# Kernel optimization log

Measured on AMD Instinct MI355X. Metric: run time of the kernel, lower is better.

Reference implementation:

```python
import jax, jax.numpy as jnp
import numpy as np

EMBED_DIM = 128
NUM_HEADS = 16
D_K = EMBED_DIM // NUM_HEADS  # 8 qubits per head
DEPTH = 2

# Sign matrix for PauliZ expectations: wire w corresponds to bit (D_K-1-w) of the
# flattened state index (wire 0 = most significant axis, torchquantum convention).
_idx = np.arange(2 ** D_K)
_SIGNS = np.stack([1.0 - 2.0 * ((_idx >> (D_K - 1 - w)) & 1) for w in range(D_K)], axis=1).astype(np.float32)  # [2^d_k, d_k]


def quantum_layer(tokens, qparams):
    """Simulate the variational circuit for a batch of tokens.
    tokens: [N, d_k] real angles; qparams: [depth, d_k] trainable RX angles.
    RX(a)RX(b)=RX(a+b) on the same wire, so encoder + all depth RX layers
    compose into a single RX per wire. Then `depth` CNOT ladders, then <Z_w>.
    """
    theta = tokens + jnp.sum(qparams, axis=0)  # [N, d_k]
    half = 0.5 * theta
    # single-qubit amplitudes after RX(theta)|0>: [cos(t/2), -i sin(t/2)]
    amp = jnp.stack([jnp.cos(half).astype(jnp.complex64),
                     (-1j) * jnp.sin(half).astype(jnp.complex64)], axis=-1)  # [N, d_k, 2]
    # build product state [N, 2, 2, ..., 2]
    state = amp[:, 0, :]
    for i in range(1, D_K):
        state = jnp.einsum('n...,nq->n...q', state, amp[:, i, :])
    # depth x CNOT ladder: CNOT(i, i+1) for i in 0..d_k-2
    for _ in range(DEPTH):
        for i in range(D_K - 1):
            c_ax = 1 + i
            c0 = jnp.take(state, 0, axis=c_ax)
            c1 = jnp.take(state, 1, axis=c_ax)
            c1 = jnp.flip(c1, axis=c_ax)  # target axis = c_ax+1, shifted by -1 after take
            state = jnp.stack([c0, c1], axis=c_ax)
    probs = (state.real ** 2 + state.imag ** 2).reshape(state.shape[0], -1)  # [N, 2^d_k]
    return probs @ jnp.asarray(_SIGNS)  # [N, d_k]


def setup_inputs() -> dict:
    key = jax.random.key(0)
    ks = jax.random.split(key, 6)
    B, S, E = 4, 512, EMBED_DIM
    scale = 1.0 / np.sqrt(E)
    return {
        'x': jax.random.normal(ks[0], (B, S, E), dtype=jnp.float32),
        'Wq': jax.random.normal(ks[1], (E, E), dtype=jnp.float32) * scale,
        'Wk': jax.random.normal(ks[2], (E, E), dtype=jnp.float32) * scale,
        'Wv': jax.random.normal(ks[3], (E, E), dtype=jnp.float32) * scale,
        'Wo': jax.random.normal(ks[4], (E, E), dtype=jnp.float32) * scale,
        'qparams': jax.random.normal(ks[5], (DEPTH, D_K), dtype=jnp.float32),
    }


def reference(x, Wq, Wk, Wv, Wo, qparams):
    B, S, E = x.shape
    H, dk = NUM_HEADS, D_K
    # linear projections (torch Linear, no bias): y = x @ W.T
    q = (x @ Wq.T).reshape(B, S, H, dk).transpose(0, 2, 1, 3)  # [B,H,S,dk]
    k = (x @ Wk.T).reshape(B, S, H, dk).transpose(0, 2, 1, 3)
    v = (x @ Wv.T).reshape(B, S, H, dk).transpose(0, 2, 1, 3)
    # batched quantum circuit over all (batch, head, seq) tokens; shared weights
    qq = quantum_layer(q.reshape(-1, dk), qparams).reshape(B, H, S, dk)
    kq = quantum_layer(k.reshape(-1, dk), qparams).reshape(B, H, S, dk)
    vq = quantum_layer(v.reshape(-1, dk), qparams).reshape(B, H, S, dk)
    scores = jnp.einsum('bhqd,bhkd->bhqk', qq, kq) / jnp.sqrt(jnp.float32(dk))
    attn = jax.nn.softmax(scores, axis=-1)  # dropout in eval mode: identity
    out = jnp.einsum('bhqk,bhkd->bhqd', attn, vq)
    out = out.transpose(0, 2, 1, 3).reshape(B, S, E)
    return out @ Wo.T
```

## Files before the change

kernel.cpp:

```cpp
#include <hip/hip_runtime.h>
#include <cmath>

#define MATSZ 262144
#define WT_OFF 0
#define QKV_OFF 65536
#define AOUT_OFF (65536 + 3 * MATSZ)

__global__ __launch_bounds__(256) void k_prep(
    const float* __restrict__ Wq, const float* __restrict__ Wk,
    const float* __restrict__ Wv, const float* __restrict__ Wo,
    float* __restrict__ ws) {
  __shared__ float s[32][33];
  const int m = blockIdx.y;
  const int tr = blockIdx.x >> 2;
  const int tc = blockIdx.x & 3;
  const float* W = (m == 0) ? Wq : (m == 1) ? Wk : (m == 2) ? Wv : Wo;
  const int lk = threadIdx.x & 31;
  const int l0 = threadIdx.x >> 5;
#pragma unroll
  for (int i = 0; i < 4; ++i) {
    int lc = l0 + i * 8;
    s[lc][lk] = W[(size_t)(tr * 32 + lc) * 128 + tc * 32 + lk];
  }
  __syncthreads();
  float* wt = ws + WT_OFF + m * 16384;
#pragma unroll
  for (int i = 0; i < 4; ++i) {
    int lkk = l0 + i * 8;
    wt[(size_t)(tc * 32 + lkk) * 128 + tr * 32 + lk] = s[lk][lkk];
  }
}

__global__ __launch_bounds__(256, 4) void k_qkvq(
    const float* __restrict__ x, const float* __restrict__ qp,
    float* __restrict__ ws) {
  __shared__ float xs[8][128];
  __shared__ float th[8][128];
  const int t = threadIdx.x;
  const int tile = blockIdx.x;
  const int m = blockIdx.y;
  {
    const float4* xg = (const float4*)(x + (size_t)tile * 1024);
    ((float4*)&xs[0][0])[t] = xg[t];
  }
  __syncthreads();
  const int cg = t & 31, rg = t >> 5;
  const float4* wt4 = (const float4*)(ws + WT_OFF + m * 16384);
  const float* xr = &xs[rg][0];
  float4 acc = make_float4(0.f, 0.f, 0.f, 0.f);
#pragma unroll 8
  for (int k = 0; k < 128; ++k) {
    float4 w = wt4[k * 32 + cg];
    float xv = xr[k];
    acc.x = fmaf(xv, w.x, acc.x);
    acc.y = fmaf(xv, w.y, acc.y);
    acc.z = fmaf(xv, w.z, acc.z);
    acc.w = fmaf(xv, w.w, acc.w);
  }
  const int j0 = (cg & 1) * 4;
  float4 cc;
  cc.x = __cosf(acc.x + qp[j0 + 0] + qp[8 + j0 + 0]);
  cc.y = __cosf(acc.y + qp[j0 + 1] + qp[8 + j0 + 1]);
  cc.z = __cosf(acc.z + qp[j0 + 2] + qp[8 + j0 + 2]);
  cc.w = __cosf(acc.w + qp[j0 + 3] + qp[8 + j0 + 3]);
  ((float4*)&th[rg][0])[cg] = cc;
  __syncthreads();
  if (t < 128) {
    const int r = t >> 4, h = t & 15;
    const float* tb = &th[r][h * 8];
    float o0 = tb[0], o1 = tb[1];
    float o2 = o0 * tb[2], o3 = o1 * tb[3];
    float o4 = o2 * tb[4], o5 = o3 * tb[5];
    float o6 = o4 * tb[6], o7 = o5 * tb[7];
    int row = tile * 8 + r;
    int b = row >> 9, s = row & 511;
    float* dst = ws + QKV_OFF + (size_t)m * MATSZ +
                 ((size_t)((b << 4) + h) * 512 + s) * 8;
    ((float4*)dst)[0] = make_float4(o0, o1, o2, o3);
    ((float4*)dst)[1] = make_float4(o4, o5, o6, o7);
  }
}

__global__ __launch_bounds__(256, 4) void k_attn(
    float* __restrict__ ws) {
  __shared__ float4 kslo[512], kshi[512], vslo[512], vshi[512];
  const int qt = blockIdx.x;
  const int bh = blockIdx.y;
  const float* qkv = ws + QKV_OFF;
  const float* Qg = qkv + (size_t)bh * 4096;
  const float4* Kg = (const float4*)(qkv + MATSZ + (size_t)bh * 4096);
  const float4* Vg = (const float4*)(qkv + 2 * (size_t)MATSZ + (size_t)bh * 4096);
  const int t = threadIdx.x;
  for (int k = t; k < 512; k += 256) {
    kslo[k] = Kg[2 * k]; kshi[k] = Kg[2 * k + 1];
    vslo[k] = Vg[2 * k]; vshi[k] = Vg[2 * k + 1];
  }
  __syncthreads();
  const int qslot = t >> 4, ko = t & 15;
  const int row0 = qt * 32 + qslot * 2;
  const float scale = 0.35355339059327373f;
  float4 qa0 = ((const float4*)(Qg + (size_t)row0 * 8))[0];
  float4 qb0 = ((const float4*)(Qg + (size_t)row0 * 8))[1];
  float4 qa1 = ((const float4*)(Qg + (size_t)(row0 + 1) * 8))[0];
  float4 qb1 = ((const float4*)(Qg + (size_t)(row0 + 1) * 8))[1];
  qa0.x *= scale; qa0.y *= scale; qa0.z *= scale; qa0.w *= scale;
  qb0.x *= scale; qb0.y *= scale; qb0.z *= scale; qb0.w *= scale;
  qa1.x *= scale; qa1.y *= scale; qa1.z *= scale; qa1.w *= scale;
  qb1.x *= scale; qb1.y *= scale; qb1.z *= scale; qb1.w *= scale;
  float l0 = 0.f, l1 = 0.f;
  float a0[8] = {0.f, 0.f, 0.f, 0.f, 0.f, 0.f, 0.f, 0.f};
  float a1[8] = {0.f, 0.f, 0.f, 0.f, 0.f, 0.f, 0.f, 0.f};
#pragma unroll 2
  for (int i = 0; i < 32; ++i) {
    int k = i * 16 + ko;
    float4 kx = kslo[k], ky = kshi[k];
    float s0 = qa0.x * kx.x + qa0.y * kx.y + qa0.z * kx.z + qa0.w * kx.w +
               qb0.x * ky.x + qb0.y * ky.y + qb0.z * ky.z + qb0.w * ky.w;
    float s1 = qa1.x * kx.x + qa1.y * kx.y + qa1.z * kx.z + qa1.w * kx.w +
               qb1.x * ky.x + qb1.y * ky.y + qb1.z * ky.z + qb1.w * ky.w;
    float p0 = __expf(s0), p1 = __expf(s1);
    float4 vx = vslo[k], vy = vshi[k];
    l0 += p0; l1 += p1;
    a0[0] = fmaf(p0, vx.x, a0[0]); a1[0] = fmaf(p1, vx.x, a1[0]);
    a0[1] = fmaf(p0, vx.y, a0[1]); a1[1] = fmaf(p1, vx.y, a1[1]);
    a0[2] = fmaf(p0, vx.z, a0[2]); a1[2] = fmaf(p1, vx.z, a1[2]);
    a0[3] = fmaf(p0, vx.w, a0[3]); a1[3] = fmaf(p1, vx.w, a1[3]);
    a0[4] = fmaf(p0, vy.x, a0[4]); a1[4] = fmaf(p1, vy.x, a1[4]);
    a0[5] = fmaf(p0, vy.y, a0[5]); a1[5] = fmaf(p1, vy.y, a1[5]);
    a0[6] = fmaf(p0, vy.z, a0[6]); a1[6] = fmaf(p1, vy.z, a1[6]);
    a0[7] = fmaf(p0, vy.w, a0[7]); a1[7] = fmaf(p1, vy.w, a1[7]);
  }
#pragma unroll
  for (int mm = 1; mm <= 8; mm <<= 1) {
    l0 += __shfl_xor(l0, mm);
    l1 += __shfl_xor(l1, mm);
#pragma unroll
    for (int j = 0; j < 8; ++j) {
      a0[j] += __shfl_xor(a0[j], mm);
      a1[j] += __shfl_xor(a1[j], mm);
    }
  }
  if (ko == 0) {
    float i0 = 1.f / l0, i1 = 1.f / l1;
    int b = bh >> 4, h = bh & 15;
    float* aout = ws + AOUT_OFF;
    float* d0 = aout + ((size_t)(b * 512 + row0)) * 128 + h * 8;
    ((float4*)d0)[0] = make_float4(a0[0] * i0, a0[1] * i0, a0[2] * i0, a0[3] * i0);
    ((float4*)d0)[1] = make_float4(a0[4] * i0, a0[5] * i0, a0[6] * i0, a0[7] * i0);
    float* d1 = d0 + 128;
    ((float4*)d1)[0] = make_float4(a1[0] * i1, a1[1] * i1, a1[2] * i1, a1[3] * i1);
    ((float4*)d1)[1] = make_float4(a1[4] * i1, a1[5] * i1, a1[6] * i1, a1[7] * i1);
  }
}

__global__ __launch_bounds__(256, 4) void k_out(
    const float* __restrict__ ws, float* __restrict__ out) {
  __shared__ float as_[4][128];
  const int t = threadIdx.x;
  const int tile = blockIdx.x;
  const float* aout = ws + AOUT_OFF;
  if (t < 128)
    ((float4*)&as_[0][0])[t] = ((const float4*)(aout + (size_t)tile * 512))[t];
  __syncthreads();
  const int cg = t & 63, rg = t >> 6;
  const float2* wt2 = (const float2*)(ws + WT_OFF + 3 * 16384);
  const float* ar = &as_[rg][0];
  float2 acc = make_float2(0.f, 0.f);
#pragma unroll 8
  for (int k = 0; k < 128; ++k) {
    float2 w = wt2[k * 64 + cg];
    float xv = ar[k];
    acc.x = fmaf(xv, w.x, acc.x);
    acc.y = fmaf(xv, w.y, acc.y);
  }
  ((float2*)(out + (size_t)(tile * 4 + rg) * 128))[cg] = acc;
}

extern "C" void kernel_launch(void* const* d_in, const int* in_sizes, int n_in,
                              void* d_out, int out_size, void* d_ws, size_t ws_size,
                              hipStream_t stream) {
  const float* x  = (const float*)d_in[0];
  const float* Wq = (const float*)d_in[1];
  const float* Wk = (const float*)d_in[2];
  const float* Wv = (const float*)d_in[3];
  const float* Wo = (const float*)d_in[4];
  const float* qp = (const float*)d_in[5];
  float* out = (float*)d_out;
  float* ws = (float*)d_ws;

  hipLaunchKernelGGL(k_prep, dim3(16, 4), dim3(256), 0, stream,
                     Wq, Wk, Wv, Wo, ws);
  hipLaunchKernelGGL(k_qkvq, dim3(256, 3), dim3(256), 0, stream, x, qp, ws);
  hipLaunchKernelGGL(k_attn, dim3(16, 64), dim3(256), 0, stream, ws);
  hipLaunchKernelGGL(k_out, dim3(512), dim3(256), 0, stream, ws, out);
}
```

Before: 49.33 us.

## Increase per-thread row blocking in projection, attention and output kernels

The QKV projection and output projection kernels now have each thread compute two rows with float4 x/weight reads, so each weight load is reused across rows and each block handles 16 rows. The quantum product chain is now computed in registers, with a lane shuffle replacing the shared-memory staging and second barrier. Attention threads now process four query rows instead of two, so K/V shared-memory reads are amortized over more rows. Grids shrink (128x3, 8x64, 128), which cuts redundant K/V staging but lowers parallelism and raises register pressure.

```diff
diff --git a/kernel.cpp b/kernel.cpp
--- a/kernel.cpp
+++ b/kernel.cpp
@@ -34,50 +34,75 @@
 __global__ __launch_bounds__(256, 4) void k_qkvq(
     const float* __restrict__ x, const float* __restrict__ qp,
     float* __restrict__ ws) {
-  __shared__ float xs[8][128];
-  __shared__ float th[8][128];
+  __shared__ float xs[16][128];
   const int t = threadIdx.x;
   const int tile = blockIdx.x;
   const int m = blockIdx.y;
   {
-    const float4* xg = (const float4*)(x + (size_t)tile * 1024);
-    ((float4*)&xs[0][0])[t] = xg[t];
+    const float4* xg = (const float4*)(x + (size_t)tile * 2048);
+    float4* xv = (float4*)&xs[0][0];
+    xv[t] = xg[t];
+    xv[t + 256] = xg[t + 256];
   }
   __syncthreads();
   const int cg = t & 31, rg = t >> 5;
   const float4* wt4 = (const float4*)(ws + WT_OFF + m * 16384);
-  const float* xr = &xs[rg][0];
-  float4 acc = make_float4(0.f, 0.f, 0.f, 0.f);
-#pragma unroll 8
-  for (int k = 0; k < 128; ++k) {
-    float4 w = wt4[k * 32 + cg];
-    float xv = xr[k];
-    acc.x = fmaf(xv, w.x, acc.x);
-    acc.y = fmaf(xv, w.y, acc.y);
-    acc.z = fmaf(xv, w.z, acc.z);
-    acc.w = fmaf(xv, w.w, acc.w);
+  const float4* xs4 = (const float4*)&xs[0][0];
+  float4 acc0 = make_float4(0.f, 0.f, 0.f, 0.f);
+  float4 acc1 = make_float4(0.f, 0.f, 0.f, 0.f);
+#pragma unroll 4
+  for (int kc = 0; kc < 32; ++kc) {
+    float4 w0 = wt4[(kc * 4 + 0) * 32 + cg];
+    float4 w1 = wt4[(kc * 4 + 1) * 32 + cg];
+    float4 w2 = wt4[(kc * 4 + 2) * 32 + cg];
+    float4 w3 = wt4[(kc * 4 + 3) * 32 + cg];
+    float4 xa = xs4[(rg * 2 + 0) * 32 + kc];
+    float4 xb = xs4[(rg * 2 + 1) * 32 + kc];
+    acc0.x = fmaf(xa.x, w0.x, acc0.x); acc0.y = fmaf(xa.x, w0.y, acc0.y);
+    acc0.z = fmaf(xa.x, w0.z, acc0.z); acc0.w = fmaf(xa.x, w0.w, acc0.w);
+    acc0.x = fmaf(xa.y, w1.x, acc0.x); acc0.y = fmaf(xa.y, w1.y, acc0.y);
+    acc0.z = fmaf(xa.y, w1.z, acc0.z); acc0.w = fmaf(xa.y, w1.w, acc0.w);
+    acc0.x = fmaf(xa.z, w2.x, acc0.x); acc0.y = fmaf(xa.z, w2.y, acc0.y);
+    acc0.z = fmaf(xa.z, w2.z, acc0.z); acc0.w = fmaf(xa.z, w2.w, acc0.w);
+    acc0.x = fmaf(xa.w, w3.x, acc0.x); acc0.y = fmaf(xa.w, w3.y, acc0.y);
+    acc0.z = fmaf(xa.w, w3.z, acc0.z); acc0.w = fmaf(xa.w, w3.w, acc0.w);
+    acc1.x = fmaf(xb.x, w0.x, acc1.x); acc1.y = fmaf(xb.x, w0.y, acc1.y);
+    acc1.z = fmaf(xb.x, w0.z, acc1.z); acc1.w = fmaf(xb.x, w0.w, acc1.w);
+    acc1.x = fmaf(xb.y, w1.x, acc1.x); acc1.y = fmaf(xb.y, w1.y, acc1.y);
+    acc1.z = fmaf(xb.y, w1.z, acc1.z); acc1.w = fmaf(xb.y, w1.w, acc1.w);
+    acc1.x = fmaf(xb.z, w2.x, acc1.x); acc1.y = fmaf(xb.z, w2.y, acc1.y);
+    acc1.z = fmaf(xb.z, w2.z, acc1.z); acc1.w = fmaf(xb.z, w2.w, acc1.w);
+    acc1.x = fmaf(xb.w, w3.x, acc1.x); acc1.y = fmaf(xb.w, w3.y, acc1.y);
+    acc1.z = fmaf(xb.w, w3.z, acc1.z); acc1.w = fmaf(xb.w, w3.w, acc1.w);
   }
   const int j0 = (cg & 1) * 4;
-  float4 cc;
-  cc.x = __cosf(acc.x + qp[j0 + 0] + qp[8 + j0 + 0]);
-  cc.y = __cosf(acc.y + qp[j0 + 1] + qp[8 + j0 + 1]);
-  cc.z = __cosf(acc.z + qp[j0 + 2] + qp[8 + j0 + 2]);
-  cc.w = __cosf(acc.w + qp[j0 + 3] + qp[8 + j0 + 3]);
-  ((float4*)&th[rg][0])[cg] = cc;
-  __syncthreads();
-  if (t < 128) {
-    const int r = t >> 4, h = t & 15;
-    const float* tb = &th[r][h * 8];
-    float o0 = tb[0], o1 = tb[1];
-    float o2 = o0 * tb[2], o3 = o1 * tb[3];
-    float o4 = o2 * tb[4], o5 = o3 * tb[5];
-    float o6 = o4 * tb[6], o7 = o5 * tb[7];
-    int row = tile * 8 + r;
+  float4 qs;
+  qs.x = qp[j0 + 0] + qp[8 + j0 + 0];
+  qs.y = qp[j0 + 1] + qp[8 + j0 + 1];
+  qs.z = qp[j0 + 2] + qp[8 + j0 + 2];
+  qs.w = qp[j0 + 3] + qp[8 + j0 + 3];
+  const int h = cg >> 1;
+  const bool hi = (cg & 1) != 0;
+#pragma unroll
+  for (int r = 0; r < 2; ++r) {
+    float4 a = (r == 0) ? acc0 : acc1;
+    float4 c;
+    c.x = __cosf(a.x + qs.x);
+    c.y = __cosf(a.y + qs.y);
+    c.z = __cosf(a.z + qs.z);
+    c.w = __cosf(a.w + qs.w);
+    float4 u;
+    u.x = c.x; u.y = c.y; u.z = c.x * c.z; u.w = c.y * c.w;
+    float gz = __shfl_xor(u.z, 1);
+    float gw = __shfl_xor(u.w, 1);
+    float mz = hi ? gz : 1.f, mw = hi ? gw : 1.f;
+    float4 o;
+    o.x = u.x * mz; o.y = u.y * mw; o.z = u.z * mz; o.w = u.w * mw;
+    int row = tile * 16 + rg * 2 + r;
     int b = row >> 9, s = row & 511;
     float* dst = ws + QKV_OFF + (size_t)m * MATSZ +
-                 ((size_t)((b << 4) + h) * 512 + s) * 8;
-    ((float4*)dst)[0] = make_float4(o0, o1, o2, o3);
-    ((float4*)dst)[1] = make_float4(o4, o5, o6, o7);
+                 ((size_t)((b << 4) + h) * 512 + s) * 8 + (hi ? 4 : 0);
+    *(float4*)dst = o;
   }
 }
 
@@ -97,83 +122,113 @@
   }
   __syncthreads();
   const int qslot = t >> 4, ko = t & 15;
-  const int row0 = qt * 32 + qslot * 2;
+  const int row0 = qt * 64 + qslot * 4;
   const float scale = 0.35355339059327373f;
-  float4 qa0 = ((const float4*)(Qg + (size_t)row0 * 8))[0];
-  float4 qb0 = ((const float4*)(Qg + (size_t)row0 * 8))[1];
-  float4 qa1 = ((const float4*)(Qg + (size_t)(row0 + 1) * 8))[0];
-  float4 qb1 = ((const float4*)(Qg + (size_t)(row0 + 1) * 8))[1];
-  qa0.x *= scale; qa0.y *= scale; qa0.z *= scale; qa0.w *= scale;
-  qb0.x *= scale; qb0.y *= scale; qb0.z *= scale; qb0.w *= scale;
-  qa1.x *= scale; qa1.y *= scale; qa1.z *= scale; qa1.w *= scale;
-  qb1.x *= scale; qb1.y *= scale; qb1.z *= scale; qb1.w *= scale;
-  float l0 = 0.f, l1 = 0.f;
-  float a0[8] = {0.f, 0.f, 0.f, 0.f, 0.f, 0.f, 0.f, 0.f};
-  float a1[8] = {0.f, 0.f, 0.f, 0.f, 0.f, 0.f, 0.f, 0.f};
+  float4 qa[4], qb[4];
+#pragma unroll
+  for (int r = 0; r < 4; ++r) {
+    qa[r] = ((const float4*)(Qg + (size_t)(row0 + r) * 8))[0];
+    qb[r] = ((const float4*)(Qg + (size_t)(row0 + r) * 8))[1];
+    qa[r].x *= scale; qa[r].y *= scale; qa[r].z *= scale; qa[r].w *= scale;
+    qb[r].x *= scale; qb[r].y *= scale; qb[r].z *= scale; qb[r].w *= scale;
+  }
+  float l[4] = {0.f, 0.f, 0.f, 0.f};
+  float a[4][8];
+#pragma unroll
+  for (int r = 0; r < 4; ++r)
+#pragma unroll
+    for (int j = 0; j < 8; ++j) a[r][j] = 0.f;
 #pragma unroll 2
   for (int i = 0; i < 32; ++i) {
     int k = i * 16 + ko;
     float4 kx = kslo[k], ky = kshi[k];
-    float s0 = qa0.x * kx.x + qa0.y * kx.y + qa0.z * kx.z + qa0.w * kx.w +
-               qb0.x * ky.x + qb0.y * ky.y + qb0.z * ky.z + qb0.w * ky.w;
-    float s1 = qa1.x * kx.x + qa1.y * kx.y + qa1.z * kx.z + qa1.w * kx.w +
-               qb1.x * ky.x + qb1.y * ky.y + qb1.z * ky.z + qb1.w * ky.w;
-    float p0 = __expf(s0), p1 = __expf(s1);
     float4 vx = vslo[k], vy = vshi[k];
-    l0 += p0; l1 += p1;
-    a0[0] = fmaf(p0, vx.x, a0[0]); a1[0] = fmaf(p1, vx.x, a1[0]);
-    a0[1] = fmaf(p0, vx.y, a0[1]); a1[1] = fmaf(p1, vx.y, a1[1]);
-    a0[2] = fmaf(p0, vx.z, a0[2]); a1[2] = fmaf(p1, vx.z, a1[2]);
-    a0[3] = fmaf(p0, vx.w, a0[3]); a1[3] = fmaf(p1, vx.w, a1[3]);
-    a0[4] = fmaf(p0, vy.x, a0[4]); a1[4] = fmaf(p1, vy.x, a1[4]);
-    a0[5] = fmaf(p0, vy.y, a0[5]); a1[5] = fmaf(p1, vy.y, a1[5]);
-    a0[6] = fmaf(p0, vy.z, a0[6]); a1[6] = fmaf(p1, vy.z, a1[6]);
-    a0[7] = fmaf(p0, vy.w, a0[7]); a1[7] = fmaf(p1, vy.w, a1[7]);
+#pragma unroll
+    for (int r = 0; r < 4; ++r) {
+      float s = qa[r].x * kx.x + qa[r].y * kx.y + qa[r].z * kx.z + qa[r].w * kx.w +
+                qb[r].x * ky.x + qb[r].y * ky.y + qb[r].z * ky.z + qb[r].w * ky.w;
+      float p = __expf(s);
+      l[r] += p;
+      a[r][0] = fmaf(p, vx.x, a[r][0]);
+      a[r][1] = fmaf(p, vx.y, a[r][1]);
+      a[r][2] = fmaf(p, vx.z, a[r][2]);
+      a[r][3] = fmaf(p, vx.w, a[r][3]);
+      a[r][4] = fmaf(p, vy.x, a[r][4]);
+      a[r][5] = fmaf(p, vy.y, a[r][5]);
+      a[r][6] = fmaf(p, vy.z, a[r][6]);
+      a[r][7] = fmaf(p, vy.w, a[r][7]);
+    }
   }
 #pragma unroll
   for (int mm = 1; mm <= 8; mm <<= 1) {
-    l0 += __shfl_xor(l0, mm);
-    l1 += __shfl_xor(l1, mm);
-#pragma unroll
-    for (int j = 0; j < 8; ++j) {
-      a0[j] += __shfl_xor(a0[j], mm);
-      a1[j] += __shfl_xor(a1[j], mm);
+#pragma unroll
+    for (int r = 0; r < 4; ++r) {
+      l[r] += __shfl_xor(l[r], mm);
+#pragma unroll
+      for (int j = 0; j < 8; ++j) a[r][j] += __shfl_xor(a[r][j], mm);
     }
   }
   if (ko == 0) {
-    float i0 = 1.f / l0, i1 = 1.f / l1;
     int b = bh >> 4, h = bh & 15;
     float* aout = ws + AOUT_OFF;
-    float* d0 = aout + ((size_t)(b * 512 + row0)) * 128 + h * 8;
-    ((float4*)d0)[0] = make_float4(a0[0] * i0, a0[1] * i0, a0[2] * i0, a0[3] * i0);
-    ((float4*)d0)[1] = make_float4(a0[4] * i0, a0[5] * i0, a0[6] * i0, a0[7] * i0);
-    float* d1 = d0 + 128;
-    ((float4*)d1)[0] = make_float4(a1[0] * i1, a1[1] * i1, a1[2] * i1, a1[3] * i1);
-    ((float4*)d1)[1] = make_float4(a1[4] * i1, a1[5] * i1, a1[6] * i1, a1[7] * i1);
+#pragma unroll
+    for (int r = 0; r < 4; ++r) {
+      float inv = 1.f / l[r];
+      float* d = aout + ((size_t)(b * 512 + row0 + r)) * 128 + h * 8;
+      ((float4*)d)[0] = make_float4(a[r][0] * inv, a[r][1] * inv,
+                                    a[r][2] * inv, a[r][3] * inv);
+      ((float4*)d)[1] = make_float4(a[r][4] * inv, a[r][5] * inv,
+                                    a[r][6] * inv, a[r][7] * inv);
+    }
   }
 }
 
 __global__ __launch_bounds__(256, 4) void k_out(
     const float* __restrict__ ws, float* __restrict__ out) {
-  __shared__ float as_[4][128];
+  __shared__ float as_[16][128];
   const int t = threadIdx.x;
   const int tile = blockIdx.x;
   const float* aout = ws + AOUT_OFF;
-  if (t < 128)
-    ((float4*)&as_[0][0])[t] = ((const float4*)(aout + (size_t)tile * 512))[t];
-  __syncthreads();
-  const int cg = t & 63, rg = t >> 6;
-  const float2* wt2 = (const float2*)(ws + WT_OFF + 3 * 16384);
-  const float* ar = &as_[rg][0];
-  float2 acc = make_float2(0.f, 0.f);
-#pragma unroll 8
-  for (int k = 0; k < 128; ++k) {
-    float2 w = wt2[k * 64 + cg];
-    float xv = ar[k];
-    acc.x = fmaf(xv, w.x, acc.x);
-    acc.y = fmaf(xv, w.y, acc.y);
-  }
-  ((float2*)(out + (size_t)(tile * 4 + rg) * 128))[cg] = acc;
+  {
+    const float4* ag = (const float4*)(aout + (size_t)tile * 2048);
+    float4* av = (float4*)&as_[0][0];
+    av[t] = ag[t];
+    av[t + 256] = ag[t + 256];
+  }
+  __syncthreads();
+  const int cg = t & 31, rg = t >> 5;
+  const float4* wt4 = (const float4*)(ws + WT_OFF + 3 * 16384);
+  const float4* as4 = (const float4*)&as_[0][0];
+  float4 acc0 = make_float4(0.f, 0.f, 0.f, 0.f);
+  float4 acc1 = make_float4(0.f, 0.f, 0.f, 0.f);
+#pragma unroll 4
+  for (int kc = 0; kc < 32; ++kc) {
+    float4 w0 = wt4[(kc * 4 + 0) * 32 + cg];
+    float4 w1 = wt4[(kc * 4 + 1) * 32 + cg];
+    float4 w2 = wt4[(kc * 4 + 2) * 32 + cg];
+    float4 w3 = wt4[(kc * 4 + 3) * 32 + cg];
+    float4 xa = as4[(rg * 2 + 0) * 32 + kc];
+    float4 xb = as4[(rg * 2 + 1) * 32 + kc];
+    acc0.x = fmaf(xa.x, w0.x, acc0.x); acc0.y = fmaf(xa.x, w0.y, acc0.y);
+    acc0.z = fmaf(xa.x, w0.z, acc0.z); acc0.w = fmaf(xa.x, w0.w, acc0.w);
+    acc0.x = fmaf(xa.y, w1.x, acc0.x); acc0.y = fmaf(xa.y, w1.y, acc0.y);
+    acc0.z = fmaf(xa.y, w1.z, acc0.z); acc0.w = fmaf(xa.y, w1.w, acc0.w);
+    acc0.x = fmaf(xa.z, w2.x, acc0.x); acc0.y = fmaf(xa.z, w2.y, acc0.y);
+    acc0.z = fmaf(xa.z, w2.z, acc0.z); acc0.w = fmaf(xa.z, w2.w, acc0.w);
+    acc0.x = fmaf(xa.w, w3.x, acc0.x); acc0.y = fmaf(xa.w, w3.y, acc0.y);
+    acc0.z = fmaf(xa.w, w3.z, acc0.z); acc0.w = fmaf(xa.w, w3.w, acc0.w);
+    acc1.x = fmaf(xb.x, w0.x, acc1.x); acc1.y = fmaf(xb.x, w0.y, acc1.y);
+    acc1.z = fmaf(xb.x, w0.z, acc1.z); acc1.w = fmaf(xb.x, w0.w, acc1.w);
+    acc1.x = fmaf(xb.y, w1.x, acc1.x); acc1.y = fmaf(xb.y, w1.y, acc1.y);
+    acc1.z = fmaf(xb.y, w1.z, acc1.z); acc1.w = fmaf(xb.y, w1.w, acc1.w);
+    acc1.x = fmaf(xb.z, w2.x, acc1.x); acc1.y = fmaf(xb.z, w2.y, acc1.y);
+    acc1.z = fmaf(xb.z, w2.z, acc1.z); acc1.w = fmaf(xb.z, w2.w, acc1.w);
+    acc1.x = fmaf(xb.w, w3.x, acc1.x); acc1.y = fmaf(xb.w, w3.y, acc1.y);
+    acc1.z = fmaf(xb.w, w3.z, acc1.z); acc1.w = fmaf(xb.w, w3.w, acc1.w);
+  }
+  const int row = tile * 16 + rg * 2;
+  ((float4*)(out + (size_t)row * 128))[cg] = acc0;
+  ((float4*)(out + (size_t)(row + 1) * 128))[cg] = acc1;
 }
 
 extern "C" void kernel_launch(void* const* d_in, const int* in_sizes, int n_in,
@@ -190,7 +245,7 @@
 
   hipLaunchKernelGGL(k_prep, dim3(16, 4), dim3(256), 0, stream,
                      Wq, Wk, Wv, Wo, ws);
-  hipLaunchKernelGGL(k_qkvq, dim3(256, 3), dim3(256), 0, stream, x, qp, ws);
-  hipLaunchKernelGGL(k_attn, dim3(16, 64), dim3(256), 0, stream, ws);
-  hipLaunchKernelGGL(k_out, dim3(512), dim3(256), 0, stream, ws, out);
-}
+  hipLaunchKernelGGL(k_qkvq, dim3(128, 3), dim3(256), 0, stream, x, qp, ws);
+  hipLaunchKernelGGL(k_attn, dim3(8, 64), dim3(256), 0, stream, ws);
+  hipLaunchKernelGGL(k_out, dim3(128), dim3(256), 0, stream, ws, out);
+}
```

New measurement: 45.96 us. 6.8% less time.
